# Kernel tuning notes

Hardware: AMD Instinct MI355X
Metric: run time of the kernel (lower is better)

The kernel has to match this reference:

```python
import jax, jax.numpy as jnp
import numpy as np

B, L, D = 8, 512, 256


def hard_sigmoid(x):
    # Keras 1.x default inner_activation for LSTM gates
    return jnp.clip(0.2 * x + 0.5, 0.0, 1.0)


def lstm_step(x_t, h, c, W, U, b):
    # gates in Keras order: i, f, g(candidate), o
    z = x_t @ W + h @ U + b  # (B, 4D)
    i, f, g, o = jnp.split(z, 4, axis=-1)
    i = hard_sigmoid(i)
    f = hard_sigmoid(f)
    g = jnp.tanh(g)
    o = hard_sigmoid(o)
    c_new = f * c + i * g
    h_new = o * jnp.tanh(c_new)
    return h_new, c_new


def setup_inputs() -> dict:
    key = jax.random.key(0)
    ks = jax.random.split(key, 10)
    s = 1.0 / np.sqrt(D)
    x = jax.random.normal(ks[0], (B, L, D), dtype=jnp.float32)
    W_r = jax.random.normal(ks[1], (D, 4 * D), dtype=jnp.float32) * s
    U_r = jax.random.normal(ks[2], (D, 4 * D), dtype=jnp.float32) * s
    b_r = jnp.zeros((4 * D,), dtype=jnp.float32)
    W_w = jax.random.normal(ks[3], (D, 4 * D), dtype=jnp.float32) * s
    U_w = jax.random.normal(ks[4], (D, 4 * D), dtype=jnp.float32) * s
    b_w = jnp.zeros((4 * D,), dtype=jnp.float32)
    W_c = jax.random.normal(ks[5], (2 * D, D), dtype=jnp.float32) * s
    b_c = jnp.zeros((D,), dtype=jnp.float32)
    return {"x": x, "W_r": W_r, "U_r": U_r, "b_r": b_r,
            "W_w": W_w, "U_w": U_w, "b_w": b_w, "W_c": W_c, "b_c": b_c}


def reference(x, W_r, U_r, b_r, W_w, U_w, b_w, W_c, b_c):
    Bb, Ll, Dd = x.shape
    h0 = jnp.zeros((Bb, Dd), dtype=x.dtype)

    # --- reader LSTM (return_sequences=True), eq. 1 ---
    def reader_step(carry, x_t):
        h, c = carry
        h, c = lstm_step(x_t, h, c, W_r, U_r, b_r)
        return (h, c), h

    _, o_seq = jax.lax.scan(reader_step, (h0, h0), jnp.swapaxes(x, 0, 1))  # (L, B, D)

    # --- compose-and-write loop, eqs. 2-6; mem_0 = x ---
    def write_step(carry, o_t):
        mem, h, c = carry  # mem: (B, L, D)
        z = jax.nn.softmax(jnp.einsum('bd,bld->bl', o_t, mem), axis=-1)  # (B, L)
        m_rt = jnp.einsum('bl,bld->bd', z, mem)                           # (B, D)
        c_t = jnp.concatenate([o_t, m_rt], axis=-1) @ W_c + b_c          # linear composer
        h_new, c_new = lstm_step(c_t, h, c, W_w, U_w, b_w)
        mem_new = mem * (1.0 - z[..., None]) + h_new[:, None, :] * z[..., None]
        return (mem_new, h_new, c_new), h_new

    (_, _, _), h_seq = jax.lax.scan(write_step, (x, h0, h0), o_seq)
    # return_mode == 'last_output'
    return h_seq[-1]
```

## Files before the change

kernel.cpp:

```cpp
#include <hip/hip_runtime.h>
#include <math.h>

#define BB 8
#define LL 512
#define DD 256
#define NG4 1024
#define WGB 32
#define WR 16
#define WU 8
#define MLD 264

typedef __attribute__((ext_vector_type(4))) float f32x4;
typedef __attribute__((ext_vector_type(4))) unsigned u32x4;

static const size_t OFF_XW    = 0;
static const size_t OFF_F     = OFF_XW + (size_t)BB*LL*NG4;
static const size_t OFF_BMW   = OFF_F + (size_t)DD*NG4;
static const size_t OFF_B2    = OFF_BMW + (size_t)DD*NG4;
static const size_t OFF_HR    = OFF_B2 + NG4;
static const size_t OFF_HW    = OFF_HR + (size_t)2*BB*DD;
static const size_t OFF_PMAX  = OFF_HW + (size_t)BB*DD;
static const size_t OFF_PSUM  = OFF_PMAX + (size_t)BB*WGB;
static const size_t OFF_RHO   = OFF_PSUM + (size_t)BB*WGB;
static const size_t OFF_PM    = OFF_RHO + (size_t)BB*WGB;
static const size_t OFF_FLAGS = OFF_PM + (size_t)BB*WGB*DD;
static const size_t TOTAL_WS  = OFF_FLAGS + BB*WGB;

__device__ __forceinline__ float hsig(float x) {
    return fminf(fmaxf(0.2f*x + 0.5f, 0.0f), 1.0f);
}

__device__ __forceinline__ void st_coh(float* p, float v) {
    __hip_atomic_store(p, v, __ATOMIC_RELAXED, __HIP_MEMORY_SCOPE_AGENT);
}
__device__ __forceinline__ float ld_coh(const float* p) {
    return __hip_atomic_load(p, __ATOMIC_RELAXED, __HIP_MEMORY_SCOPE_AGENT);
}
__device__ __forceinline__ void st_coh_u(unsigned* p, unsigned v) {
    __hip_atomic_store(p, v, __ATOMIC_RELAXED, __HIP_MEMORY_SCOPE_AGENT);
}

__device__ __forceinline__ u32x4 ld_coh_u4(const unsigned* p) {
    u32x4 r;
    asm volatile("global_load_dwordx4 %0, %1, off sc0 sc1\n\t"
                 "s_waitcnt vmcnt(0)"
                 : "=&v"(r) : "v"(p) : "memory");
    return r;
}

__device__ __forceinline__ void wave_poll(const unsigned* flb, unsigned target, int tid) {
    if ((tid & 63) < 8) {
        const unsigned* fp = flb + (tid & 63)*4;
        for (;;) {
            u32x4 v = ld_coh_u4(fp);
            if (v[0] >= target && v[1] >= target && v[2] >= target && v[3] >= target) break;
        }
    }
}

__device__ __forceinline__ void ld_pm8(
    const f32x4* p0, const f32x4* p1, const f32x4* p2, const f32x4* p3,
    const f32x4* p4, const f32x4* p5, const f32x4* p6, const f32x4* p7,
    f32x4& a0, f32x4& a1, f32x4& a2, f32x4& a3,
    f32x4& a4, f32x4& a5, f32x4& a6, f32x4& a7)
{
    asm volatile(
        "global_load_dwordx4 %0, %8, off sc0 sc1\n\t"
        "global_load_dwordx4 %1, %9, off sc0 sc1\n\t"
        "global_load_dwordx4 %2, %10, off sc0 sc1\n\t"
        "global_load_dwordx4 %3, %11, off sc0 sc1\n\t"
        "global_load_dwordx4 %4, %12, off sc0 sc1\n\t"
        "global_load_dwordx4 %5, %13, off sc0 sc1\n\t"
        "global_load_dwordx4 %6, %14, off sc0 sc1\n\t"
        "global_load_dwordx4 %7, %15, off sc0 sc1\n\t"
        "s_waitcnt vmcnt(0)"
        : "=&v"(a0), "=&v"(a1), "=&v"(a2), "=&v"(a3),
          "=&v"(a4), "=&v"(a5), "=&v"(a6), "=&v"(a7)
        : "v"(p0), "v"(p1), "v"(p2), "v"(p3),
          "v"(p4), "v"(p5), "v"(p6), "v"(p7)
        : "memory");
}

template<int TM, int TN, int TK>
__global__ void __launch_bounds__(256) gemm_nn(
    const float* __restrict__ A, int lda,
    const float* __restrict__ Bmat, int ldb,
    const float* __restrict__ bias,
    float* __restrict__ C, int ldc,
    int M, int N, int K)
{
    __shared__ float As[TK][TM];
    __shared__ float Bs[TK][TN];
    const int m0 = blockIdx.y * TM, n0 = blockIdx.x * TN;
    const int tid = threadIdx.x;
    const int tx = tid % (TN/4);
    const int ty = tid / (TN/4);
    float acc[4][4] = {};
    for (int k0 = 0; k0 < K; k0 += TK) {
        {
            const int e = tid*4;
            const int m = e / TK, k = e % TK;
            const float4 v = *reinterpret_cast<const float4*>(&A[(size_t)(m0+m)*lda + k0 + k]);
            As[k+0][m] = v.x; As[k+1][m] = v.y; As[k+2][m] = v.z; As[k+3][m] = v.w;
        }
        {
            const int e = tid*4;
            const int k = e / TN, n = e % TN;
            const float4 v = *reinterpret_cast<const float4*>(&Bmat[(size_t)(k0+k)*ldb + n0 + n]);
            Bs[k][n+0] = v.x; Bs[k][n+1] = v.y; Bs[k][n+2] = v.z; Bs[k][n+3] = v.w;
        }
        __syncthreads();
        #pragma unroll
        for (int kk = 0; kk < TK; ++kk) {
            float a[4], bv[4];
            #pragma unroll
            for (int i = 0; i < 4; ++i) a[i] = As[kk][ty*4+i];
            #pragma unroll
            for (int j = 0; j < 4; ++j) bv[j] = Bs[kk][tx*4+j];
            #pragma unroll
            for (int i = 0; i < 4; ++i)
                #pragma unroll
                for (int j = 0; j < 4; ++j) acc[i][j] += a[i]*bv[j];
        }
        __syncthreads();
    }
    #pragma unroll
    for (int i = 0; i < 4; ++i) {
        const int m = m0 + ty*4 + i;
        #pragma unroll
        for (int j = 0; j < 4; ++j) {
            const int n = n0 + tx*4 + j;
            C[(size_t)m*ldc + n] = acc[i][j] + (bias ? bias[n] : 0.0f);
        }
    }
}

__global__ void __launch_bounds__(256) b2_kernel(
    const float* __restrict__ bc, const float* __restrict__ Ww,
    const float* __restrict__ bw, float* __restrict__ B2)
{
    const int n = blockIdx.x*256 + threadIdx.x;
    float a = bw[n];
    for (int k = 0; k < DD; ++k) a += bc[k]*Ww[(size_t)k*NG4 + n];
    B2[n] = a;
}

__global__ void __launch_bounds__(256) fused_kernel(
    const float* __restrict__ XW, const float* __restrict__ Fw,
    const float* __restrict__ Bm, const float* __restrict__ B2,
    const float* __restrict__ Ur, const float* __restrict__ Uw,
    const float* __restrict__ x,
    float* __restrict__ HR, float* __restrict__ HWb,
    float* __restrict__ PMAX, float* __restrict__ PSUM, float* __restrict__ RHO,
    float* __restrict__ PM,
    unsigned* __restrict__ flags, float* __restrict__ out)
{
    extern __shared__ float sm[];
    float* Urs  = sm;
    float* Uws  = Urs + 8192;
    float* Fs   = Uws + 8192;
    float* Bms  = Fs + 8192;
    float* mems = Bms + 8192;
    float* hr2  = mems + WR*MLD;
    float* hw   = hr2 + 512;
    float* ms   = hw + 256;
    float* zredR= ms + 256;
    float* zredW= zredR + 256;
    float* red4 = zredW + 256;
    float* xws  = red4 + 1024;
    float* b2s  = xws + 32;
    float* zrs  = b2s + 32;
    float* zws  = zrs + 32;
    float* fwS  = zws + 32;
    float* d1   = fwS + 32;
    float* zp   = d1 + 16;
    float* esx  = zp + 16;
    float* wv   = esx + 16;
    float* cr   = wv + 16;
    float* cw   = cr + 8;
    float* misc = cw + 8;

    const int b   = (int)blockIdx.x & 7;
    const int wg  = (int)blockIdx.x >> 3;
    const int tid = threadIdx.x;
    const int R0  = wg*WR;
    const int U0  = wg*WU;
    const int gc32 = (tid>>3)*DD + U0 + (tid&7);

    for (int it = 0; it < 32; ++it) {
        const int e = it*256 + tid;
        const int k = e >> 5, cl = e & 31;
        const int gc = (cl>>3)*DD + U0 + (cl&7);
        Urs[k*32+cl] = Ur[(size_t)k*NG4 + gc];
        Uws[k*32+cl] = Uw[(size_t)k*NG4 + gc];
        Fs [k*32+cl] = Fw[(size_t)k*NG4 + gc];
        Bms[k*32+cl] = Bm[(size_t)k*NG4 + gc];
    }
    if (tid < 32) b2s[tid] = B2[gc32];
    for (int r = 0; r < WR; ++r)
        mems[r*MLD + tid] = x[((size_t)b*LL + R0 + r)*DD + tid];
    {
        const size_t base = (size_t)b*LL*NG4;
        const float zi = XW[base + tid];
        const float zg = XW[base + 512 + tid];
        const float zo = XW[base + 768 + tid];
        const float c0 = hsig(zi)*tanhf(zg);
        hr2[tid] = hsig(zo)*tanhf(c0);
        hr2[256 + tid] = 0.f;
        if (tid >= U0 && tid < U0+WU) cr[tid-U0] = c0;
    }
    if (tid < 16) { zp[tid] = 0.f; d1[tid] = 0.f; esx[tid] = 0.f; }
    if (tid < 8)  cw[tid] = 0.f;
    if (tid < 4)  misc[tid] = 0.f;
    __syncthreads();

    unsigned* flb = &flags[b*WGB];

    for (int s = 0; s <= LL; ++s) {
        const bool doW = (s >= 1);
        float* hrN_s = hr2 + (s&1)*256;
        float* hrO_s = hr2 + ((s+1)&1)*256;

        float xw_r = 0.f;
        if (s <= LL-2 && tid < 32) xw_r = XW[((size_t)b*LL + s + 1)*NG4 + gc32];
        float hw_r = 0.f, rho_r = 0.f;
        if (s >= 2) {
            hw_r = ld_coh(&HWb[b*DD + tid]);
            if (tid < 32) rho_r = ld_coh(&RHO[b*WGB + tid]);
        }
        hw[tid] = hw_r;
        __syncthreads();

        if (s <= LL-2 && tid < 32) xws[tid] = xw_r;

        if (tid < 32) {
            float d2 = rho_r;
            #pragma unroll
            for (int off = 16; off; off >>= 1) d2 += __shfl_xor(d2, off, 32);
            if (doW && tid < 16) {
                const float zpv = zp[tid];
                const float sc  = (1.f - zpv)*d1[tid] + zpv*d2;
                float m = sc;
                #pragma unroll
                for (int off = 8; off; off >>= 1) m = fmaxf(m, __shfl_xor(m, off, 16));
                const float e = __expf(sc - m);
                esx[tid] = e;
                wv[tid]  = e*(1.f - zpv);
                float sum = e, bp = e*zpv;
                #pragma unroll
                for (int off = 8; off; off >>= 1) {
                    sum += __shfl_xor(sum, off, 16);
                    bp  += __shfl_xor(bp,  off, 16);
                }
                if (tid == 0) {
                    misc[2] = bp;
                    st_coh(&PMAX[b*WGB + wg], m);
                    st_coh(&PSUM[b*WGB + wg], sum);
                }
            }
        }
        __syncthreads();

        if (doW) {
            float p = misc[2]*hw_r;
            #pragma unroll
            for (int r = 0; r < WR; ++r) p += wv[r]*mems[r*MLD + tid];
            st_coh(&PM[((size_t)b*WGB + wg)*DD + tid], p);
        }

        asm volatile("s_waitcnt vmcnt(0)" ::: "memory");
        __syncthreads();
        const unsigned tgt1 = 2u*(unsigned)s + 1u;
        if (tid == 0) st_coh_u(&flb[wg], tgt1);
        if (s >= 2) {
            #pragma unroll
            for (int r = 0; r < WR; ++r) {
                const float z = zp[r];
                float* mp = &mems[r*MLD + tid];
                *mp = *mp*(1.f - z) + hw_r*z;
            }
        }
        if (doW) {
            const int kc = tid >> 5, cl = tid & 31, k0 = kc*32;
            float a = 0.f;
            #pragma unroll 8
            for (int k = k0; k < k0+32; ++k)
                a += hw[k]*Uws[k*32+cl] + hrO_s[k]*Fs[k*32+cl];
            zredW[tid] = a;
        }
        wave_poll(flb, tgt1, tid);

        float hrN_r = 0.f;
        if (s >= 1 && s <= LL-1) hrN_r = ld_coh(&HR[((size_t)(s&1))*BB*DD + b*DD + tid]);
        float pmx_r = 0.f, ps_r = 0.f;
        if (doW && tid < 32) {
            pmx_r = ld_coh(&PMAX[b*WGB + tid]);
            ps_r  = ld_coh(&PSUM[b*WGB + tid]);
        }
        f32x4 a0,a1,a2,a3,a4,a5,a6,a7;
        const int w0 = tid >> 6, dq = tid & 63;
        if (doW) {
            const float* pmb = PM + (size_t)b*WGB*DD;
            ld_pm8((const f32x4*)(pmb + (w0+ 0)*DD) + dq, (const f32x4*)(pmb + (w0+ 4)*DD) + dq,
                   (const f32x4*)(pmb + (w0+ 8)*DD) + dq, (const f32x4*)(pmb + (w0+12)*DD) + dq,
                   (const f32x4*)(pmb + (w0+16)*DD) + dq, (const f32x4*)(pmb + (w0+20)*DD) + dq,
                   (const f32x4*)(pmb + (w0+24)*DD) + dq, (const f32x4*)(pmb + (w0+28)*DD) + dq,
                   a0,a1,a2,a3,a4,a5,a6,a7);
        }
        if (s >= 1 && s <= LL-1) hrN_s[tid] = hrN_r;
        if (doW && tid < 32) {
            float g = pmx_r;
            #pragma unroll
            for (int off = 16; off; off >>= 1) g = fmaxf(g, __shfl_xor(g, off, 32));
            const float fw = __expf(pmx_r - g);
            float S = ps_r*fw;
            #pragma unroll
            for (int off = 16; off; off >>= 1) S += __shfl_xor(S, off, 32);
            fwS[tid] = fw;
            if (tid == 0)  misc[1] = 1.f/S;
            if (tid == wg) misc[0] = fw/S;
        }
        __syncthreads();

        if (s <= LL-2) {
            const int kc = tid >> 5, cl = tid & 31, k0 = kc*32;
            float a = 0.f;
            #pragma unroll 8
            for (int k = k0; k < k0+32; ++k) a += hrN_s[k]*Urs[k*32+cl];
            zredR[tid] = a;
        }
        if (doW) {
            f32x4 acc = a0*fwS[w0];
            acc += a1*fwS[w0+4];  acc += a2*fwS[w0+8];
            acc += a3*fwS[w0+12]; acc += a4*fwS[w0+16];
            acc += a5*fwS[w0+20]; acc += a6*fwS[w0+24];
            acc += a7*fwS[w0+28];
            *(f32x4*)(red4 + w0*DD + dq*4) = acc;
        }
        __syncthreads();
        if (doW) {
            ms[tid] = (red4[tid] + red4[DD+tid] + red4[2*DD+tid] + red4[3*DD+tid]) * misc[1];
            if (tid < 16) zp[tid] = esx[tid]*misc[0];
        }
        __syncthreads();
        if (doW) {
            const int kc = tid >> 5, cl = tid & 31, k0 = kc*32;
            float a = zredW[tid];
            #pragma unroll 8
            for (int k = k0; k < k0+32; ++k) a += ms[k]*Bms[k*32+cl];
            zredW[tid] = a;
        }
        __syncthreads();
        if (tid < 32) {
            if (doW) {
                float z = b2s[tid];
                #pragma unroll
                for (int q = 0; q < 8; ++q) z += zredW[q*32 + tid];
                zws[tid] = z;
            }
            if (s <= LL-2) {
                float z = xws[tid];
                #pragma unroll
                for (int q = 0; q < 8; ++q) z += zredR[q*32 + tid];
                zrs[tid] = z;
            }
        }
        __syncthreads();

        if (doW && tid < 8) {
            const float ig = hsig(zws[tid]);
            const float fg = hsig(zws[8+tid]);
            const float gg = tanhf(zws[16+tid]);
            const float og = hsig(zws[24+tid]);
            const float c  = fg*cw[tid] + ig*gg;
            cw[tid] = c;
            const float h = og*tanhf(c);
            st_coh(&HWb[b*DD + U0 + tid], h);
            if (s < LL) {
                float rr = h * hrN_s[U0 + tid];
                rr += __shfl_down(rr, 4, 8);
                rr += __shfl_down(rr, 2, 8);
                rr += __shfl_down(rr, 1, 8);
                if (tid == 0) st_coh(&RHO[b*WGB + wg], rr);
            }
            if (s == LL) out[b*DD + U0 + tid] = h;
        }
        if (s <= LL-2 && tid < 8) {
            const float ig = hsig(zrs[tid]);
            const float fg = hsig(zrs[8+tid]);
            const float gg = tanhf(zrs[16+tid]);
            const float og = hsig(zrs[24+tid]);
            const float c  = fg*cr[tid] + ig*gg;
            cr[tid] = c;
            st_coh(&HR[((size_t)((s+1)&1))*BB*DD + b*DD + U0 + tid], og*tanhf(c));
        }

        if (s < LL) {
            asm volatile("s_waitcnt vmcnt(0)" ::: "memory");
            __syncthreads();
            const unsigned tgt2 = 2u*(unsigned)s + 2u;
            if (tid == 0) st_coh_u(&flb[wg], tgt2);
            {
                const int r = tid >> 4, j = tid & 15;
                float a = 0.f;
                const float* mrow = mems + r*MLD;
                #pragma unroll 4
                for (int d = j; d < DD; d += 16) a += hrN_s[d]*mrow[d];
                #pragma unroll
                for (int off = 8; off; off >>= 1) a += __shfl_down(a, off, 16);
                if (j == 0) d1[r] = a;
            }
            wave_poll(flb, tgt2, tid);
        }
    }
}

extern "C" void kernel_launch(void* const* d_in, const int* in_sizes, int n_in,
                              void* d_out, int out_size, void* d_ws, size_t ws_size,
                              hipStream_t stream) {
    const float* x   = (const float*)d_in[0];
    const float* W_r = (const float*)d_in[1];
    const float* U_r = (const float*)d_in[2];
    const float* b_r = (const float*)d_in[3];
    const float* W_w = (const float*)d_in[4];
    const float* U_w = (const float*)d_in[5];
    const float* b_w = (const float*)d_in[6];
    const float* W_c = (const float*)d_in[7];
    const float* b_c = (const float*)d_in[8];
    (void)in_sizes; (void)n_in;

    if (ws_size < TOTAL_WS * sizeof(float)) return;

    float* ws   = (float*)d_ws;
    float* XW   = ws + OFF_XW;
    float* Fmat = ws + OFF_F;
    float* Bmw  = ws + OFF_BMW;
    float* B2   = ws + OFF_B2;
    float* HR   = ws + OFF_HR;
    float* HWb  = ws + OFF_HW;
    float* PMAX = ws + OFF_PMAX;
    float* PSUM = ws + OFF_PSUM;
    float* RHO  = ws + OFF_RHO;
    float* PM   = ws + OFF_PM;
    unsigned* flags = (unsigned*)(ws + OFF_FLAGS);

    const int FUSED_LDS = 39800 * 4;
    hipFuncSetAttribute((const void*)fused_kernel, hipFuncAttributeMaxDynamicSharedMemorySize, FUSED_LDS);

    hipMemsetAsync(flags, 0, BB*WGB*sizeof(unsigned), stream);

    dim3 blk(256);
    gemm_nn<64,64,16><<<dim3(NG4/64, (BB*LL)/64), blk, 0, stream>>>(
        x, DD, W_r, NG4, b_r, XW, NG4, BB*LL, NG4, DD);
    gemm_nn<64,64,16><<<dim3(NG4/64, DD/64), blk, 0, stream>>>(
        W_c, DD, W_w, NG4, nullptr, Fmat, NG4, DD, NG4, DD);
    gemm_nn<64,64,16><<<dim3(NG4/64, DD/64), blk, 0, stream>>>(
        W_c + (size_t)DD*DD, DD, W_w, NG4, nullptr, Bmw, NG4, DD, NG4, DD);
    b2_kernel<<<dim3(NG4/256), blk, 0, stream>>>(b_c, W_w, b_w, B2);
    fused_kernel<<<dim3(BB*WGB), blk, FUSED_LDS, stream>>>(
        XW, Fmat, Bmw, B2, U_r, U_w, x, HR, HWb, PMAX, PSUM, RHO, PM, flags, (float*)d_out);
}
```

Measured before the change: 3.947 ms.

## Replace flag barriers with tagged value/step pairs for inter-workgroup sync

Replaces the two per-step grid-wide flag barriers with data words that carry their own step tag (value+tag stored as one dwordx2/dwordx4), so consumers poll directly on the data they need. Softmax max/sum partials are packed with a step tag into one chunk per workgroup. This removes the full all-to-all barrier waits and lets workgroups proceed as soon as their specific inputs are ready, at the cost of more polling traffic and relying on atomicity of wide stores. The PM buffer is still read without an explicit tag, so its ordering relies on the chunk store issued after a vmcnt wait.

Result: faster. 3.784 ms (-4.1%).

```diff
diff --git a/kernel.cpp b/kernel.cpp
--- a/kernel.cpp
+++ b/kernel.cpp
@@ -11,20 +11,19 @@
 #define MLD 264
 
 typedef __attribute__((ext_vector_type(4))) float f32x4;
+typedef __attribute__((ext_vector_type(2))) unsigned u32x2;
 typedef __attribute__((ext_vector_type(4))) unsigned u32x4;
 
 static const size_t OFF_XW    = 0;
 static const size_t OFF_F     = OFF_XW + (size_t)BB*LL*NG4;
 static const size_t OFF_BMW   = OFF_F + (size_t)DD*NG4;
 static const size_t OFF_B2    = OFF_BMW + (size_t)DD*NG4;
-static const size_t OFF_HR    = OFF_B2 + NG4;
-static const size_t OFF_HW    = OFF_HR + (size_t)2*BB*DD;
-static const size_t OFF_PMAX  = OFF_HW + (size_t)BB*DD;
-static const size_t OFF_PSUM  = OFF_PMAX + (size_t)BB*WGB;
-static const size_t OFF_RHO   = OFF_PSUM + (size_t)BB*WGB;
-static const size_t OFF_PM    = OFF_RHO + (size_t)BB*WGB;
-static const size_t OFF_FLAGS = OFF_PM + (size_t)BB*WGB*DD;
-static const size_t TOTAL_WS  = OFF_FLAGS + BB*WGB;
+static const size_t OFF_HRT   = OFF_B2 + NG4;
+static const size_t OFF_HWT   = OFF_HRT + (size_t)2*BB*DD*2;
+static const size_t OFF_RHOT  = OFF_HWT + (size_t)BB*DD*2;
+static const size_t OFF_CHUNK = OFF_RHOT + (size_t)BB*WGB*2;
+static const size_t OFF_PM    = OFF_CHUNK + (size_t)BB*WGB*4;
+static const size_t TOTAL_WS  = OFF_PM + (size_t)BB*WGB*DD;
 
 __device__ __forceinline__ float hsig(float x) {
     return fminf(fmaxf(0.2f*x + 0.5f, 0.0f), 1.0f);
@@ -33,31 +32,28 @@
 __device__ __forceinline__ void st_coh(float* p, float v) {
     __hip_atomic_store(p, v, __ATOMIC_RELAXED, __HIP_MEMORY_SCOPE_AGENT);
 }
-__device__ __forceinline__ float ld_coh(const float* p) {
-    return __hip_atomic_load(p, __ATOMIC_RELAXED, __HIP_MEMORY_SCOPE_AGENT);
-}
-__device__ __forceinline__ void st_coh_u(unsigned* p, unsigned v) {
-    __hip_atomic_store(p, v, __ATOMIC_RELAXED, __HIP_MEMORY_SCOPE_AGENT);
-}
-
-__device__ __forceinline__ u32x4 ld_coh_u4(const unsigned* p) {
-    u32x4 r;
-    asm volatile("global_load_dwordx4 %0, %1, off sc0 sc1\n\t"
-                 "s_waitcnt vmcnt(0)"
+__device__ __forceinline__ void st_pair(unsigned* p, float v, unsigned tag) {
+    u32x2 d; d[0] = __float_as_uint(v); d[1] = tag;
+    asm volatile("global_store_dwordx2 %0, %1, off sc0 sc1" :: "v"(p), "v"(d) : "memory");
+}
+__device__ __forceinline__ u32x2 ld_pair(const unsigned* p) {
+    u32x2 r;
+    asm volatile("global_load_dwordx2 %0, %1, off sc0 sc1\n\ts_waitcnt vmcnt(0)"
                  : "=&v"(r) : "v"(p) : "memory");
     return r;
 }
-
-__device__ __forceinline__ void wave_poll(const unsigned* flb, unsigned target, int tid) {
-    if ((tid & 63) < 8) {
-        const unsigned* fp = flb + (tid & 63)*4;
-        for (;;) {
-            u32x4 v = ld_coh_u4(fp);
-            if (v[0] >= target && v[1] >= target && v[2] >= target && v[3] >= target) break;
-        }
-    }
-}
-
+__device__ __forceinline__ float poll_pair(const unsigned* p, unsigned tag) {
+    for (;;) {
+        u32x2 r = ld_pair(p);
+        if (r[1] >= tag) return __uint_as_float(r[0]);
+    }
+}
+__device__ __forceinline__ u32x4 ld_chunk(const unsigned* p) {
+    u32x4 r;
+    asm volatile("global_load_dwordx4 %0, %1, off sc0 sc1\n\ts_waitcnt vmcnt(0)"
+                 : "=&v"(r) : "v"(p) : "memory");
+    return r;
+}
 __device__ __forceinline__ void ld_pm8(
     const f32x4* p0, const f32x4* p1, const f32x4* p2, const f32x4* p3,
     const f32x4* p4, const f32x4* p5, const f32x4* p6, const f32x4* p7,
@@ -150,10 +146,9 @@
     const float* __restrict__ Bm, const float* __restrict__ B2,
     const float* __restrict__ Ur, const float* __restrict__ Uw,
     const float* __restrict__ x,
-    float* __restrict__ HR, float* __restrict__ HWb,
-    float* __restrict__ PMAX, float* __restrict__ PSUM, float* __restrict__ RHO,
-    float* __restrict__ PM,
-    unsigned* __restrict__ flags, float* __restrict__ out)
+    unsigned* __restrict__ HRT, unsigned* __restrict__ HWT,
+    unsigned* __restrict__ RHOT, unsigned* __restrict__ CHUNK,
+    float* __restrict__ PM, float* __restrict__ out)
 {
     extern __shared__ float sm[];
     float* Urs  = sm;
@@ -214,25 +209,24 @@
     if (tid < 4)  misc[tid] = 0.f;
     __syncthreads();
 
-    unsigned* flb = &flags[b*WGB];
-
     for (int s = 0; s <= LL; ++s) {
         const bool doW = (s >= 1);
         float* hrN_s = hr2 + (s&1)*256;
         float* hrO_s = hr2 + ((s+1)&1)*256;
 
-        float xw_r = 0.f;
-        if (s <= LL-2 && tid < 32) xw_r = XW[((size_t)b*LL + s + 1)*NG4 + gc32];
+        if (s <= LL-2 && tid < 32)
+            xws[tid] = XW[((size_t)b*LL + s + 1)*NG4 + gc32];
+
         float hw_r = 0.f, rho_r = 0.f;
         if (s >= 2) {
-            hw_r = ld_coh(&HWb[b*DD + tid]);
-            if (tid < 32) rho_r = ld_coh(&RHO[b*WGB + tid]);
+            hw_r = poll_pair(HWT + 2*((size_t)b*DD + tid), (unsigned)(s-1));
+            if (tid < 32)
+                rho_r = poll_pair(RHOT + 2*(b*WGB + tid), (unsigned)(s-1));
         }
         hw[tid] = hw_r;
         __syncthreads();
 
-        if (s <= LL-2 && tid < 32) xws[tid] = xw_r;
-
+        float ck_m = 0.f, ck_s = 0.f;
         if (tid < 32) {
             float d2 = rho_r;
             #pragma unroll
@@ -252,11 +246,7 @@
                     sum += __shfl_xor(sum, off, 16);
                     bp  += __shfl_xor(bp,  off, 16);
                 }
-                if (tid == 0) {
-                    misc[2] = bp;
-                    st_coh(&PMAX[b*WGB + wg], m);
-                    st_coh(&PSUM[b*WGB + wg], sum);
-                }
+                if (tid == 0) { misc[2] = bp; ck_m = m; ck_s = sum; }
             }
         }
         __syncthreads();
@@ -267,11 +257,14 @@
             for (int r = 0; r < WR; ++r) p += wv[r]*mems[r*MLD + tid];
             st_coh(&PM[((size_t)b*WGB + wg)*DD + tid], p);
         }
-
         asm volatile("s_waitcnt vmcnt(0)" ::: "memory");
         __syncthreads();
-        const unsigned tgt1 = 2u*(unsigned)s + 1u;
-        if (tid == 0) st_coh_u(&flb[wg], tgt1);
+        if (doW && tid == 0) {
+            u32x4 d; d[0] = __float_as_uint(ck_m); d[1] = __float_as_uint(ck_s);
+            d[2] = (unsigned)s; d[3] = 0u;
+            unsigned* cp = CHUNK + 4*(b*WGB + wg);
+            asm volatile("global_store_dwordx4 %0, %1, off sc0 sc1" :: "v"(cp), "v"(d) : "memory");
+        }
         if (s >= 2) {
             #pragma unroll
             for (int r = 0; r < WR; ++r) {
@@ -288,16 +281,21 @@
                 a += hw[k]*Uws[k*32+cl] + hrO_s[k]*Fs[k*32+cl];
             zredW[tid] = a;
         }
-        wave_poll(flb, tgt1, tid);
 
         float hrN_r = 0.f;
-        if (s >= 1 && s <= LL-1) hrN_r = ld_coh(&HR[((size_t)(s&1))*BB*DD + b*DD + tid]);
+        if (s >= 1 && s <= LL-1)
+            hrN_r = poll_pair(HRT + 2*(((size_t)(s&1)*BB + b)*DD + tid), (unsigned)s);
         float pmx_r = 0.f, ps_r = 0.f;
         if (doW && tid < 32) {
-            pmx_r = ld_coh(&PMAX[b*WGB + tid]);
-            ps_r  = ld_coh(&PSUM[b*WGB + tid]);
-        }
-        f32x4 a0,a1,a2,a3,a4,a5,a6,a7;
+            const unsigned* cp = CHUNK + 4*(b*WGB + tid);
+            u32x4 ck;
+            do { ck = ld_chunk(cp); } while (ck[2] < (unsigned)s);
+            pmx_r = __uint_as_float(ck[0]); ps_r = __uint_as_float(ck[1]);
+        }
+        if (s >= 1 && s <= LL-1) hrN_s[tid] = hrN_r;
+        __syncthreads();
+
+        f32x4 a0={},a1={},a2={},a3={},a4={},a5={},a6={},a7={};
         const int w0 = tid >> 6, dq = tid & 63;
         if (doW) {
             const float* pmb = PM + (size_t)b*WGB*DD;
@@ -307,7 +305,6 @@
                    (const f32x4*)(pmb + (w0+24)*DD) + dq, (const f32x4*)(pmb + (w0+28)*DD) + dq,
                    a0,a1,a2,a3,a4,a5,a6,a7);
         }
-        if (s >= 1 && s <= LL-1) hrN_s[tid] = hrN_r;
         if (doW && tid < 32) {
             float g = pmx_r;
             #pragma unroll
@@ -320,8 +317,6 @@
             if (tid == 0)  misc[1] = 1.f/S;
             if (tid == wg) misc[0] = fw/S;
         }
-        __syncthreads();
-
         if (s <= LL-2) {
             const int kc = tid >> 5, cl = tid & 31, k0 = kc*32;
             float a = 0.f;
@@ -329,6 +324,8 @@
             for (int k = k0; k < k0+32; ++k) a += hrN_s[k]*Urs[k*32+cl];
             zredR[tid] = a;
         }
+        __syncthreads();
+
         if (doW) {
             f32x4 acc = a0*fwS[w0];
             acc += a1*fwS[w0+4];  acc += a2*fwS[w0+8];
@@ -375,13 +372,13 @@
             const float c  = fg*cw[tid] + ig*gg;
             cw[tid] = c;
             const float h = og*tanhf(c);
-            st_coh(&HWb[b*DD + U0 + tid], h);
+            st_pair(HWT + 2*((size_t)b*DD + U0 + tid), h, (unsigned)s);
             if (s < LL) {
                 float rr = h * hrN_s[U0 + tid];
                 rr += __shfl_down(rr, 4, 8);
                 rr += __shfl_down(rr, 2, 8);
                 rr += __shfl_down(rr, 1, 8);
-                if (tid == 0) st_coh(&RHO[b*WGB + wg], rr);
+                if (tid == 0) st_pair(RHOT + 2*(b*WGB + wg), rr, (unsigned)s);
             }
             if (s == LL) out[b*DD + U0 + tid] = h;
         }
@@ -392,25 +389,18 @@
             const float og = hsig(zrs[24+tid]);
             const float c  = fg*cr[tid] + ig*gg;
             cr[tid] = c;
-            st_coh(&HR[((size_t)((s+1)&1))*BB*DD + b*DD + U0 + tid], og*tanhf(c));
-        }
-
+            st_pair(HRT + 2*(((size_t)((s+1)&1)*BB + b)*DD + U0 + tid),
+                    og*tanhf(c), (unsigned)(s+1));
+        }
         if (s < LL) {
-            asm volatile("s_waitcnt vmcnt(0)" ::: "memory");
-            __syncthreads();
-            const unsigned tgt2 = 2u*(unsigned)s + 2u;
-            if (tid == 0) st_coh_u(&flb[wg], tgt2);
-            {
-                const int r = tid >> 4, j = tid & 15;
-                float a = 0.f;
-                const float* mrow = mems + r*MLD;
-                #pragma unroll 4
-                for (int d = j; d < DD; d += 16) a += hrN_s[d]*mrow[d];
-                #pragma unroll
-                for (int off = 8; off; off >>= 1) a += __shfl_down(a, off, 16);
-                if (j == 0) d1[r] = a;
-            }
-            wave_poll(flb, tgt2, tid);
+            const int r = tid >> 4, j = tid & 15;
+            float a = 0.f;
+            const float* mrow = mems + r*MLD;
+            #pragma unroll 4
+            for (int d = j; d < DD; d += 16) a += hrN_s[d]*mrow[d];
+            #pragma unroll
+            for (int off = 8; off; off >>= 1) a += __shfl_down(a, off, 16);
+            if (j == 0) d1[r] = a;
         }
     }
 }
@@ -436,18 +426,16 @@
     float* Fmat = ws + OFF_F;
     float* Bmw  = ws + OFF_BMW;
     float* B2   = ws + OFF_B2;
-    float* HR   = ws + OFF_HR;
-    float* HWb  = ws + OFF_HW;
-    float* PMAX = ws + OFF_PMAX;
-    float* PSUM = ws + OFF_PSUM;
-    float* RHO  = ws + OFF_RHO;
+    unsigned* HRT   = (unsigned*)(ws + OFF_HRT);
+    unsigned* HWT   = (unsigned*)(ws + OFF_HWT);
+    unsigned* RHOT  = (unsigned*)(ws + OFF_RHOT);
+    unsigned* CHUNK = (unsigned*)(ws + OFF_CHUNK);
     float* PM   = ws + OFF_PM;
-    unsigned* flags = (unsigned*)(ws + OFF_FLAGS);
 
     const int FUSED_LDS = 39800 * 4;
     hipFuncSetAttribute((const void*)fused_kernel, hipFuncAttributeMaxDynamicSharedMemorySize, FUSED_LDS);
 
-    hipMemsetAsync(flags, 0, BB*WGB*sizeof(unsigned), stream);
+    hipMemsetAsync(HRT, 0, (OFF_PM - OFF_HRT)*sizeof(float), stream);
 
     dim3 blk(256);
     gemm_nn<64,64,16><<<dim3(NG4/64, (BB*LL)/64), blk, 0, stream>>>(
@@ -458,5 +446,5 @@
         W_c + (size_t)DD*DD, DD, W_w, NG4, nullptr, Bmw, NG4, DD, NG4, DD);
     b2_kernel<<<dim3(NG4/256), blk, 0, stream>>>(b_c, W_w, b_w, B2);
     fused_kernel<<<dim3(BB*WGB), blk, FUSED_LDS, stream>>>(
-        XW, Fmat, Bmw, B2, U_r, U_w, x, HR, HWb, PMAX, PSUM, RHO, PM, flags, (float*)d_out);
-}
+        XW, Fmat, Bmw, B2, U_r, U_w, x, HRT, HWT, RHOT, CHUNK, PM, (float*)d_out);
+}
```
